# Kernel optimization log

Measured on AMD Instinct MI355X. Metric: run time of the kernel, lower is better.

Reference implementation:

```python
import jax, jax.numpy as jnp
import numpy as np

N = 262144
D = 128      # input_dim
H = 64       # hidden size of each group head
G = 4        # num_groups
P = 4        # num_phases


def setup_inputs() -> dict:
    key = jax.random.key(0)
    k1, k2, k3, k4, k5, k6, k7 = jax.random.split(key, 7)
    h_int = jax.random.normal(k1, (N, D), dtype=jnp.float32)
    group_ids = jax.random.randint(k2, (N,), 0, G, dtype=jnp.int64)
    feasible_mask = jax.random.randint(k3, (N, P), 0, 2, dtype=jnp.int32).astype(jnp.bool_)
    # Stacked per-group head params: Linear(D->H), ReLU, Linear(H->P)
    W1 = jax.random.normal(k4, (G, D, H), dtype=jnp.float32) / np.sqrt(D)
    b1 = jax.random.normal(k5, (G, H), dtype=jnp.float32) * 0.01
    W2 = jax.random.normal(k6, (G, H, P), dtype=jnp.float32) / np.sqrt(H)
    b2 = jax.random.normal(k7, (G, P), dtype=jnp.float32) * 0.01
    return {"h_int": h_int, "group_ids": group_ids, "feasible_mask": feasible_mask,
            "W1": W1, "b1": b1, "W2": W2, "b2": b2}


def reference(h_int, group_ids, feasible_mask, W1, b1, W2, b2):
    # Dense grouped-GEMM: evaluate every head on every row, then select by group id.
    # hidden: [N, G, H]
    hidden = jax.nn.relu(jnp.einsum('nd,gdh->ngh', h_int, W1) + b1[None])
    # all_logits: [N, G, P]
    all_logits = jnp.einsum('ngh,ghp->ngp', hidden, W2) + b2[None]
    # select the row's own group head -> [N, P]
    gid = group_ids.astype(jnp.int32)[:, None, None]
    logits = jnp.take_along_axis(all_logits, gid, axis=1)[:, 0, :]
    logits = jnp.where(feasible_mask, logits, jnp.float32(-1e9))
    return jax.nn.softmax(logits, axis=-1)
```

## Files before the change

kernel.cpp:

```cpp
#include <hip/hip_runtime.h>
#include <hip/hip_bf16.h>
#include <cstdint>

#define NROWS 262144
#define DIM 128

typedef float f32x4 __attribute__((ext_vector_type(4)));
typedef short s16x8 __attribute__((ext_vector_type(8)));
typedef unsigned short u16x8 __attribute__((ext_vector_type(8)));
typedef unsigned int u32x4 __attribute__((ext_vector_type(4)));

__device__ __forceinline__ unsigned short cvbf(float f){
  unsigned u = __float_as_uint(f);
  return (unsigned short)((u + 0x8000u) >> 16);
}

__device__ __forceinline__ void ldsload16(const void* gp, void* lp){
  __builtin_amdgcn_global_load_lds((const __attribute__((address_space(1))) void*)gp,
                                   (__attribute__((address_space(3))) void*)lp,
                                   16, 0, 0);
}

__global__ void prep_kernel(const float* __restrict__ W1, const float* __restrict__ W2,
                            const void* __restrict__ gids_raw, const void* __restrict__ mask_raw,
                            unsigned char* __restrict__ ws){
  int tid = threadIdx.x, bid = blockIdx.x;
  if (bid < 16){
    int chunk = bid*256 + tid;
    int n    = chunk >> 4;
    int kb16 = chunk & 15;
    int d0   = kb16 * 8;
    int g = n >> 6, h = n & 63;
    u16x8 v;
#pragma unroll
    for (int j=0;j<8;++j) v[j] = cvbf(W1[((g*DIM) + d0 + j)*64 + h]);
    unsigned off = (unsigned)n*256 + (((unsigned)kb16*16) ^ (((unsigned)(n&7))<<4));
    *(u16x8*)(ws + off) = v;
  } else {
#pragma unroll
    for (int i=0;i<16;++i){
      int el = tid + i*256;
      int t  = el >> 6;
      int e  = el & 63;
      int g = t >> 4, p = t & 15;
      int h = (e & 32) | ((e & 4) << 2) | ((e >> 1) & 12) | (e & 3);
      float f = (p < 4) ? W2[(g*64 + h)*4 + p] : 0.0f;
      unsigned off = 65536u + (unsigned)t*128 + (((unsigned)(e*2)) ^ (((unsigned)(t&7))<<4));
      *(unsigned short*)(ws + off) = cvbf(f);
    }
    if (tid < 64){
      const int* g32 = (const int*)gids_raw;
      int accg = 0;
#pragma unroll
      for (int i=0;i<8;++i) accg |= g32[(tid*8 + i)*2 + 1];
      const unsigned char* m8 = (const unsigned char*)mask_raw;
      int accm = 0;
#pragma unroll
      for (int i=0;i<16;++i){
        int off = tid*16 + i;
        if (off & 3) accm |= m8[off];
      }
      unsigned long long bg = __ballot(accg != 0);
      unsigned long long bm = __ballot(accm != 0);
      if (tid == 0){
        *(int*)(ws + 73728) = (bg == 0ull) ? 1 : 0;
        *(int*)(ws + 73732) = (bm == 0ull) ? 2 : 0;
      }
    }
  }
}

#define LDS_W2T 65536
#define LDS_B1  (65536+8192)
#define PERM_OFF   (65536+8192+1024)
#define HIST_OFF   (PERM_OFF+1280)
#define CUR_OFF    (HIST_OFF+16)
#define NUNITS_OFF (CUR_OFF+16)
#define UG_OFF     (NUNITS_OFF+16)
#define UP_OFF     (UG_OFF+80)
#define LDS_TOTAL  (UP_OFF+80)

__global__ __launch_bounds__(256, 2)
void actor_kernel(const float* __restrict__ X, const int* __restrict__ gids,
                  const unsigned char* __restrict__ fmask,
                  const float* __restrict__ b1, const float* __restrict__ b2,
                  const unsigned char* __restrict__ ws, float* __restrict__ out){
  __shared__ char smem[LDS_TOTAL];
  const int tid  = threadIdx.x;
  const int wave = tid >> 6, lane = tid & 63;
  const int q    = lane >> 4, rS = lane & 15;
  const int swzA = (rS & 7) << 4;

  const int gshift = *(const int*)(ws + 73728);
  const int mshift = *(const int*)(ws + 73732);

  short* perm = (short*)(smem + PERM_OFF);
  int* hist = (int*)(smem + HIST_OFF);
  int* cur  = (int*)(smem + CUR_OFF);
  int* ug   = (int*)(smem + UG_OFF);
  int* up   = (int*)(smem + UP_OFF);

#pragma unroll
  for (int i=0;i<16;++i){
    int off = i*4096 + wave*1024;
    ldsload16(ws + off + lane*16, smem + off);
  }
#pragma unroll
  for (int i=0;i<2;++i){
    int off = i*4096 + wave*1024;
    ldsload16(ws + 65536 + off + lane*16, smem + LDS_W2T + off);
  }
  if (wave == 0)
    ldsload16((const unsigned char*)b1 + lane*16, smem + LDS_B1);

  const long base = (long)blockIdx.x * 512;
  if (tid < 4) hist[tid] = 0;
#pragma unroll
  for (int i = 0; i < 3; ++i){
    int e = tid + i*256;
    if (e < 640) perm[e] = -1;
  }
  __syncthreads();
  const int g0 = gids[(size_t)(base + tid) << gshift] & 3;
  const int g1 = gids[(size_t)(base + 256 + tid) << gshift] & 3;
  atomicAdd(&hist[g0], 1);
  atomicAdd(&hist[g1], 1);
  __syncthreads();
  if (tid == 0){
    int s = 0, n = 0;
    for (int g=0; g<4; ++g){
      cur[g] = s;
      int padded = ((hist[g] + 31) >> 5) << 5;
      for (int k=0; k<padded; k+=32){ ug[n] = g; up[n] = s + k; ++n; }
      s += padded;
    }
    *(int*)(smem + NUNITS_OFF) = n;
  }
  __syncthreads();
  { int p0 = atomicAdd(&cur[g0], 1); perm[p0] = (short)tid;
    int p1 = atomicAdd(&cur[g1], 1); perm[p1] = (short)(256 + tid); }
  __syncthreads();
  const int nunits = *(const int*)(smem + NUNITS_OFF);

  const f32x4 z = (f32x4){0.f,0.f,0.f,0.f};

#pragma unroll 1
  for (int uu = 0; uu < 5; ++uu){
    const int idx = wave + uu*4;
    if (idx >= nunits) break;
    const int g   = ug[idx];
    const int pos = up[idx];
    const int r0l = perm[pos + rS];
    const int r1l = perm[pos + 16 + rS];
    const long rr0 = base + (r0l < 0 ? 0 : r0l);
    const long rr1 = base + (r1l < 0 ? 0 : r1l);

    u32x4 mb0, mb1;
    if (mshift){
      mb0 = *(const u32x4*)(fmask + rr0*16);
      mb1 = *(const u32x4*)(fmask + rr1*16);
    } else {
      unsigned w0 = *(const unsigned*)(fmask + rr0*4);
      unsigned w1 = *(const unsigned*)(fmask + rr1*4);
      mb0[0]=w0&0xffu; mb0[1]=(w0>>8)&0xffu; mb0[2]=(w0>>16)&0xffu; mb0[3]=w0>>24;
      mb1[0]=w1&0xffu; mb1[1]=(w1>>8)&0xffu; mb1[2]=(w1>>16)&0xffu; mb1[3]=w1>>24;
    }

    f32x4 xb[2][4][2];
    {
      const float* xp0 = X + rr0 * DIM + q*8;
      const float* xp1 = X + rr1 * DIM + q*8;
#pragma unroll
      for (int k=0;k<4;++k){
        xb[0][k][0] = *(const f32x4*)(xp0 + k*32);
        xb[0][k][1] = *(const f32x4*)(xp0 + k*32 + 4);
        xb[1][k][0] = *(const f32x4*)(xp1 + k*32);
        xb[1][k][1] = *(const f32x4*)(xp1 + k*32 + 4);
      }
    }
    __builtin_amdgcn_sched_barrier(0);

    s16x8 bfr[2][4];
#pragma unroll
    for (int nt=0;nt<2;++nt)
#pragma unroll
      for (int k=0;k<4;++k){
        s16x8 v;
#pragma unroll
        for (int j=0;j<4;++j){ v[j] = (short)cvbf(xb[nt][k][0][j]); v[j+4] = (short)cvbf(xb[nt][k][1][j]); }
        bfr[nt][k] = v;
      }
    __builtin_amdgcn_sched_barrier(0);

    f32x4 acc2[2];
#pragma unroll
    for (int pp=0;pp<2;++pp){
      const int p = 2*g + pp;
      f32x4 aA0, aA1, aB0, aB1;
#pragma unroll
      for (int k=0;k<4;++k){
        const s16x8 sA = *(const s16x8*)(smem + ((2*p  )*16 + rS)*256 + ((k*64 + q*16) ^ swzA));
        const s16x8 sB = *(const s16x8*)(smem + ((2*p+1)*16 + rS)*256 + ((k*64 + q*16) ^ swzA));
        aA0 = __builtin_amdgcn_mfma_f32_16x16x32_bf16(sA, bfr[0][k], (k==0)? z : aA0, 0,0,0);
        aA1 = __builtin_amdgcn_mfma_f32_16x16x32_bf16(sA, bfr[1][k], (k==0)? z : aA1, 0,0,0);
        aB0 = __builtin_amdgcn_mfma_f32_16x16x32_bf16(sB, bfr[0][k], (k==0)? z : aB0, 0,0,0);
        aB1 = __builtin_amdgcn_mfma_f32_16x16x32_bf16(sB, bfr[1][k], (k==0)? z : aB1, 0,0,0);
      }
      const f32x4 b1A = *(const f32x4*)(smem + LDS_B1 + (2*p  )*64 + q*16);
      const f32x4 b1B = *(const f32x4*)(smem + LDS_B1 + (2*p+1)*64 + q*16);
      const s16x8 af = *(const s16x8*)(smem + LDS_W2T + (g*16 + rS)*128
                                       + ((pp*64 + q*16) ^ swzA));
      {
        f32x4 vA = aA0 + b1A, vB = aB0 + b1B;
#pragma unroll
        for (int j=0;j<4;++j){ vA[j] = vA[j] > 0.f ? vA[j] : 0.f; vB[j] = vB[j] > 0.f ? vB[j] : 0.f; }
        s16x8 hf;
#pragma unroll
        for (int j=0;j<4;++j){ hf[j] = (short)cvbf(vA[j]); hf[j+4] = (short)cvbf(vB[j]); }
        acc2[0] = __builtin_amdgcn_mfma_f32_16x16x32_bf16(af, hf, pp ? acc2[0] : z, 0,0,0);
      }
      {
        f32x4 vA = aA1 + b1A, vB = aB1 + b1B;
#pragma unroll
        for (int j=0;j<4;++j){ vA[j] = vA[j] > 0.f ? vA[j] : 0.f; vB[j] = vB[j] > 0.f ? vB[j] : 0.f; }
        s16x8 hf;
#pragma unroll
        for (int j=0;j<4;++j){ hf[j] = (short)cvbf(vA[j]); hf[j+4] = (short)cvbf(vB[j]); }
        acc2[1] = __builtin_amdgcn_mfma_f32_16x16x32_bf16(af, hf, pp ? acc2[1] : z, 0,0,0);
      }
      __builtin_amdgcn_sched_barrier(0);
    }

    const f32x4 bs = *(const f32x4*)(b2 + g*4);
#pragma unroll
    for (int nt=0;nt<2;++nt){
      u32x4 mb = nt ? mb1 : mb0;
      f32x4 lv = acc2[nt];
      f32x4 li;
#pragma unroll
      for (int p=0;p<4;++p)
        li[p] = mb[p] ? (lv[p] + bs[p]) : -1e9f;
      float m = fmaxf(fmaxf(li[0],li[1]), fmaxf(li[2],li[3]));
      f32x4 e;
#pragma unroll
      for (int p=0;p<4;++p) e[p] = __expf(li[p] - m);
      float inv = 1.0f / (e[0]+e[1]+e[2]+e[3]);
      f32x4 o;
#pragma unroll
      for (int p=0;p<4;++p) o[p] = e[p] * inv;
      int rl = nt ? r1l : r0l;
      long rr = nt ? rr1 : rr0;
      if (q == 0 && rl >= 0)
        *(f32x4*)(out + rr*4) = o;
    }
  }
}

extern "C" void kernel_launch(void* const* d_in, const int* in_sizes, int n_in,
                              void* d_out, int out_size, void* d_ws, size_t ws_size,
                              hipStream_t stream){
  const float* X  = (const float*)d_in[0];
  const void*  gi = d_in[1];
  const void*  fm = d_in[2];
  const float* W1 = (const float*)d_in[3];
  const float* b1 = (const float*)d_in[4];
  const float* W2 = (const float*)d_in[5];
  const float* b2 = (const float*)d_in[6];
  unsigned char* ws = (unsigned char*)d_ws;
  float* out = (float*)d_out;

  prep_kernel<<<dim3(17), dim3(256), 0, stream>>>(W1, W2, gi, fm, ws);
  actor_kernel<<<dim3(512), dim3(256), 0, stream>>>(X, (const int*)gi,
                                                    (const unsigned char*)fm,
                                                    b1, b2, ws, out);
}
```

Before: 41.08 us.

## Split each row chunk's groups across two blocks to halve per-block LDS weights

The grid doubles to 1024 blocks. Each 512-row chunk is now handled by two blocks, each owning one pair of groups. A block stages only its pair's half of W1 (32KB instead of 64KB), plus its half of W2 and b1, into LDS, and only permutes and processes rows belonging to its groups. This cuts per-block LDS footprint and staging latency and lets more blocks run at once, at the cost of every block reading all group ids and building the histogram twice per chunk.

```diff
diff --git a/kernel.cpp b/kernel.cpp
--- a/kernel.cpp
+++ b/kernel.cpp
@@ -70,15 +70,15 @@
   }
 }
 
-#define LDS_W2T 65536
-#define LDS_B1  (65536+8192)
-#define PERM_OFF   (65536+8192+1024)
-#define HIST_OFF   (PERM_OFF+1280)
-#define CUR_OFF    (HIST_OFF+16)
+#define W2T_OFF   32768
+#define B1_OFF    36864
+#define PERM_OFF  37376
+#define HIST_OFF  (PERM_OFF+1280)
+#define CUR_OFF   (HIST_OFF+16)
 #define NUNITS_OFF (CUR_OFF+16)
-#define UG_OFF     (NUNITS_OFF+16)
-#define UP_OFF     (UG_OFF+80)
-#define LDS_TOTAL  (UP_OFF+80)
+#define UG_OFF    (NUNITS_OFF+16)
+#define UP_OFF    (UG_OFF+80)
+#define LDS_TOTAL (UP_OFF+80)
 
 __global__ __launch_bounds__(256, 2)
 void actor_kernel(const float* __restrict__ X, const int* __restrict__ gids,
@@ -91,6 +91,9 @@
   const int q    = lane >> 4, rS = lane & 15;
   const int swzA = (rS & 7) << 4;
 
+  const int pair = blockIdx.x >> 9;
+  const long base = (long)(blockIdx.x & 511) * 512;
+
   const int gshift = *(const int*)(ws + 73728);
   const int mshift = *(const int*)(ws + 73732);
 
@@ -101,19 +104,15 @@
   int* up   = (int*)(smem + UP_OFF);
 
 #pragma unroll
-  for (int i=0;i<16;++i){
+  for (int i=0;i<8;++i){
     int off = i*4096 + wave*1024;
-    ldsload16(ws + off + lane*16, smem + off);
-  }
-#pragma unroll
-  for (int i=0;i<2;++i){
-    int off = i*4096 + wave*1024;
-    ldsload16(ws + 65536 + off + lane*16, smem + LDS_W2T + off);
-  }
-  if (wave == 0)
-    ldsload16((const unsigned char*)b1 + lane*16, smem + LDS_B1);
-
-  const long base = (long)blockIdx.x * 512;
+    ldsload16(ws + pair*32768 + off + lane*16, smem + off);
+  }
+  ldsload16(ws + 65536 + pair*4096 + wave*1024 + lane*16,
+            smem + W2T_OFF + wave*1024 + lane*16);
+  if (wave == 0 && lane < 32)
+    ldsload16((const unsigned char*)b1 + pair*512 + lane*16, smem + B1_OFF + lane*16);
+
   if (tid < 4) hist[tid] = 0;
 #pragma unroll
   for (int i = 0; i < 3; ++i){
@@ -128,17 +127,18 @@
   __syncthreads();
   if (tid == 0){
     int s = 0, n = 0;
-    for (int g=0; g<4; ++g){
+    for (int gg=0; gg<2; ++gg){
+      int g = pair*2 + gg;
       cur[g] = s;
       int padded = ((hist[g] + 31) >> 5) << 5;
-      for (int k=0; k<padded; k+=32){ ug[n] = g; up[n] = s + k; ++n; }
+      for (int k=0; k<padded; k+=32){ ug[n] = gg; up[n] = s + k; ++n; }
       s += padded;
     }
     *(int*)(smem + NUNITS_OFF) = n;
   }
   __syncthreads();
-  { int p0 = atomicAdd(&cur[g0], 1); perm[p0] = (short)tid;
-    int p1 = atomicAdd(&cur[g1], 1); perm[p1] = (short)(256 + tid); }
+  if ((g0 >> 1) == pair){ int p0 = atomicAdd(&cur[g0], 1); perm[p0] = (short)tid; }
+  if ((g1 >> 1) == pair){ int p1 = atomicAdd(&cur[g1], 1); perm[p1] = (short)(256 + tid); }
   __syncthreads();
   const int nunits = *(const int*)(smem + NUNITS_OFF);
 
@@ -148,7 +148,7 @@
   for (int uu = 0; uu < 5; ++uu){
     const int idx = wave + uu*4;
     if (idx >= nunits) break;
-    const int g   = ug[idx];
+    const int gg  = ug[idx];
     const int pos = up[idx];
     const int r0l = perm[pos + rS];
     const int r1l = perm[pos + 16 + rS];
@@ -195,7 +195,7 @@
     f32x4 acc2[2];
 #pragma unroll
     for (int pp=0;pp<2;++pp){
-      const int p = 2*g + pp;
+      const int p = 2*gg + pp;
       f32x4 aA0, aA1, aB0, aB1;
 #pragma unroll
       for (int k=0;k<4;++k){
@@ -206,9 +206,9 @@
         aB0 = __builtin_amdgcn_mfma_f32_16x16x32_bf16(sB, bfr[0][k], (k==0)? z : aB0, 0,0,0);
         aB1 = __builtin_amdgcn_mfma_f32_16x16x32_bf16(sB, bfr[1][k], (k==0)? z : aB1, 0,0,0);
       }
-      const f32x4 b1A = *(const f32x4*)(smem + LDS_B1 + (2*p  )*64 + q*16);
-      const f32x4 b1B = *(const f32x4*)(smem + LDS_B1 + (2*p+1)*64 + q*16);
-      const s16x8 af = *(const s16x8*)(smem + LDS_W2T + (g*16 + rS)*128
+      const f32x4 b1A = *(const f32x4*)(smem + B1_OFF + (2*p  )*64 + q*16);
+      const f32x4 b1B = *(const f32x4*)(smem + B1_OFF + (2*p+1)*64 + q*16);
+      const s16x8 af = *(const s16x8*)(smem + W2T_OFF + (gg*16 + rS)*128
                                        + ((pp*64 + q*16) ^ swzA));
       {
         f32x4 vA = aA0 + b1A, vB = aB0 + b1B;
@@ -231,7 +231,7 @@
       __builtin_amdgcn_sched_barrier(0);
     }
 
-    const f32x4 bs = *(const f32x4*)(b2 + g*4);
+    const f32x4 bs = *(const f32x4*)(b2 + (pair*2 + gg)*4);
 #pragma unroll
     for (int nt=0;nt<2;++nt){
       u32x4 mb = nt ? mb1 : mb0;
@@ -270,7 +270,7 @@
   float* out = (float*)d_out;
 
   prep_kernel<<<dim3(17), dim3(256), 0, stream>>>(W1, W2, gi, fm, ws);
-  actor_kernel<<<dim3(512), dim3(256), 0, stream>>>(X, (const int*)gi,
-                                                    (const unsigned char*)fm,
-                                                    b1, b2, ws, out);
-}
+  actor_kernel<<<dim3(1024), dim3(256), 0, stream>>>(X, (const int*)gi,
+                                                     (const unsigned char*)fm,
+                                                     b1, b2, ws, out);
+}
```

After: 44.17 us. 1.08x slower.
